# Performance work log

Hardware: AMD Instinct MI355X
Metric: run time of the kernel (lower is better)

## Reference

```python
import jax, jax.numpy as jnp
import numpy as np

B, L, K = 16, 512, 30          # proteins, residues per protein, kNN neighbors
N = B * L
H, FC = 32, 3                  # h_channels, frame_channels
C = H + FC                     # fused sphere channels (35)
HEADS, AC, VC = 8, 16, 8       # heads, alpha channels (H//2), value channels (H//4)
RBF_N, POS_N = 16, 16
EF = RBF_N + POS_N

# idealized backbone atom positions (N, CA, C) in the local residue frame
IDEAL_BB = np.array([[-0.525, 1.363, 0.0], [0.0, 0.0, 0.0], [1.526, 0.0, 0.0]], dtype=np.float32)
# cartesian (x,y,z) -> real-SH l=1 ordering (y,z,x)
P_SH = np.array([[0., 1., 0.], [0., 0., 1.], [1., 0., 0.]], dtype=np.float32)


def _knn_edges(trans):
    # per-chain brute-force kNN (chains are contiguous blocks of length L)
    X = trans.reshape(B, L, 3)
    d2 = jnp.sum((X[:, :, None, :] - X[:, None, :, :]) ** 2, axis=-1)  # [B,L,L]
    d2 = d2 + jnp.eye(L, dtype=d2.dtype) * 1e9                          # exclude self
    _, idx = jax.lax.top_k(-d2, K)                                      # [B,L,K]
    off = (jnp.arange(B) * L)[:, None, None]
    src = (idx + off).reshape(-1)              # neighbor (edge_index[0])
    tgt = jnp.repeat(jnp.arange(N), K)         # center   (edge_index[1])
    return src, tgt


def _edge_rot_mat(vec):
    # rotation aligning the edge vector with the y axis (eSCN init_edge_rot_mat style)
    nx = vec / (jnp.linalg.norm(vec, axis=-1, keepdims=True) + 1e-12)
    ref = jnp.where(jnp.abs(nx[:, :1]) < 0.9,
                    jnp.array([1., 0., 0.], dtype=vec.dtype),
                    jnp.array([0., 0., 1.], dtype=vec.dtype))
    nz = jnp.cross(nx, ref)
    nz = nz / (jnp.linalg.norm(nz, axis=-1, keepdims=True) + 1e-12)
    ny = jnp.cross(nx, nz)
    ny = ny / (jnp.linalg.norm(ny, axis=-1, keepdims=True) + 1e-12)
    return jnp.stack([nz, nx, ny], axis=-2)  # [E,3,3]


def _rbf(d, d_min=0.0, d_max=20.0, count=RBF_N):
    mu = jnp.linspace(d_min, d_max, count)
    sigma = (d_max - d_min) / count
    return jnp.exp(-(((d[:, None] - mu) / sigma) ** 2))


def _pos_emb(src, tgt, num=POS_N):
    d = (src - tgt).astype(jnp.float32)
    freq = jnp.exp(jnp.arange(0, num, 2, dtype=jnp.float32) * (-np.log(10000.0) / num))
    ang = d[:, None] * freq
    return jnp.concatenate([jnp.cos(ang), jnp.sin(ang)], axis=-1)


def _forward(rots, trans, node_emb, batch, x_mask, noising_mask,
             W_alpha, a_vec, W_v, W_o, W_g, W_2):
    src, tgt = _knn_edges(trans)
    vec = trans[src] - trans[tgt]
    dist = jnp.linalg.norm(vec, axis=-1)
    valid = jnp.isfinite(dist) & (dist > 1e-3)  # edge_select, applied as mask

    R = _edge_rot_mat(vec)
    P = jnp.asarray(P_SH)
    D1 = jnp.einsum('ij,ejk,lk->eil', P, R, P)  # l=1 Wigner in real-SH basis [E,3,3]

    edge_features = jnp.concatenate([_rbf(dist), _pos_emb(src, tgt)], axis=-1)  # [E,32]

    # fuse node features with backbone frame atoms and editability flag
    frame_atoms = jnp.einsum('nij,aj->nai', rots, jnp.asarray(IDEAL_BB))  # [N,3atoms,3xyz]
    editable = noising_mask & (~x_mask)
    emb = jnp.zeros((N, 4, C), dtype=node_emb.dtype)
    emb = emb.at[:, :, :H].set(node_emb)
    emb = emb.at[:, 1:4, H:].set(jnp.swapaxes(frame_atoms, -1, -2))
    emb = emb.at[:, 0, C - 1].set(editable.astype(node_emb.dtype))

    # gather + rotate source features into edge frames
    xs = emb[src]                                                   # [E,4,C]
    xs_rot = jnp.concatenate([xs[:, :1], jnp.einsum('eij,ejc->eic', D1, xs[:, 1:])], axis=1)

    # invariant attention logits (l=0 of rotated src, l=0 of tgt, edge feats)
    inv = jnp.concatenate([xs_rot[:, 0], emb[tgt, 0], edge_features], axis=-1)  # [E,102]
    hdn = jax.nn.silu(inv @ W_alpha).reshape(-1, HEADS, AC)
    logits = jax.nn.leaky_relu(jnp.einsum('ehk,hk->eh', hdn, a_vec), 0.2)
    logits = jnp.where(valid[:, None], logits, -1e9)

    # segment softmax over incoming edges of each target node
    mx = jax.lax.stop_gradient(jax.ops.segment_max(logits, tgt, num_segments=N))
    ex = jnp.exp(logits - mx[tgt]) * valid[:, None].astype(logits.dtype)
    den = jax.ops.segment_sum(ex, tgt, num_segments=N)
    alpha = ex / (den[tgt] + 1e-9)                                  # [E,HEADS]

    # equivariant values, attention-weighted, rotate back, scatter
    v = (xs_rot @ W_v).reshape(-1, 4, HEADS, VC)
    m = (v * alpha[:, None, :, None]).reshape(-1, 4, HEADS * VC)
    m = jnp.concatenate([m[:, :1], jnp.einsum('eji,ejc->eic', D1, m[:, 1:])], axis=1)  # D^T
    agg = jax.ops.segment_sum(m, tgt, num_segments=N)               # [N,4,64]

    y = agg @ W_o                                                    # [N,4,H]
    gate = jax.nn.silu(y[:, 0] @ W_g)                                # invariant gating FFN
    return (y * gate[:, None, :]) @ W_2                              # [N,4,H]


def setup_inputs():
    key = jax.random.key(0)
    ks = jax.random.split(key, 12)
    rots = jax.vmap(lambda m: jnp.linalg.qr(m)[0])(jax.random.normal(ks[0], (N, 3, 3)))
    trans = jax.random.normal(ks[1], (N, 3)) * 10.0
    node_emb = jax.random.normal(ks[2], (N, 4, H))
    batch = jnp.repeat(jnp.arange(B, dtype=jnp.int32), L)
    x_mask = jax.random.randint(ks[3], (N,), 0, 2).astype(bool)
    noising_mask = jax.random.randint(ks[4], (N,), 0, 2).astype(bool)
    s = lambda k, sh, fan: jax.random.normal(k, sh) / np.sqrt(fan)
    return dict(rots=rots, trans=trans, node_emb=node_emb, batch=batch,
                x_mask=x_mask, noising_mask=noising_mask,
                W_alpha=s(ks[5], (2 * C + EF, HEADS * AC), 2 * C + EF),
                a_vec=s(ks[6], (HEADS, AC), AC),
                W_v=s(ks[7], (C, HEADS * VC), C),
                W_o=s(ks[8], (HEADS * VC, H), HEADS * VC),
                W_g=s(ks[9], (H, H), H),
                W_2=s(ks[10], (H, H), H))


def reference(rots, trans, node_emb, batch, x_mask, noising_mask,
              W_alpha, a_vec, W_v, W_o, W_g, W_2):
    return _forward(rots, trans, node_emb, batch, x_mask, noising_mask,
                    W_alpha, a_vec, W_v, W_o, W_g, W_2)
```

## Files before the change

### kernel.cpp

```cpp
#include <hip/hip_runtime.h>
#include <cstdint>

#define B_ 16
#define L_ 512
#define N_ 8192
#define K_ 30
#define E_ (N_*K_)
#define H_ 32
#define C_ 35

typedef uint16_t u16;
typedef uint32_t u32;
typedef unsigned long long u64;

static __device__ __forceinline__ float ldf(const void* p, int i, int bf) {
    return bf ? __uint_as_float(((u32)((const u16*)p)[i]) << 16)
              : ((const float*)p)[i];
}
static __device__ __forceinline__ float bfu16(u16 x) {
    return __uint_as_float(((u32)x) << 16);
}
static __device__ __forceinline__ int ldmask(const void* p, int i, int mode) {
    if (mode == 0) return ((const unsigned char*)p)[i] != 0;
    if (mode == 2) return ((const u32*)p)[2*i] != 0;
    return ((const u32*)p)[i] != 0;
}
static __device__ __forceinline__ u16 f2bf(float f) {
    u32 x = __float_as_uint(f);
    u32 r = x + 0x7FFFu + ((x >> 16) & 1u);
    return (u16)(r >> 16);
}
static __device__ __forceinline__ float fsilu(float x) {
    return x * __builtin_amdgcn_rcpf(1.f + __expf(-x));
}

static __device__ __forceinline__ int detect_bf(const void* tr, int lane) {
    const u16* p = (const u16*)tr;
    int cnt = 0;
    for (int i = lane; i < 256; i += 64) {
        u16 v = p[2 * i];
        int e = (v >> 7) & 0xFF;
        if ((e >= 100 && e <= 141) || (v & 0x7FFFu) == 0) cnt++;
    }
    #pragma unroll
    for (int d = 1; d < 64; d <<= 1) cnt += __shfl_xor(cnt, d, 64);
    return cnt >= 192;
}
static __device__ __forceinline__ int detect_mm(const void* xmv, int lane) {
    const u32* xm = (const u32*)xmv;
    int anyBig = 0, oddNZ = 0;
    for (int i = lane; i < 1024; i += 64) {
        u32 w = xm[i];
        if (w & ~1u) anyBig = 1;
        if ((i & 1) && w) oddNZ = 1;
    }
    #pragma unroll
    for (int d = 1; d < 64; d <<= 1) {
        anyBig |= __shfl_xor(anyBig, d, 64);
        oddNZ  |= __shfl_xor(oddNZ, d, 64);
    }
    return anyBig ? 0 : (oddNZ ? 1 : 2);
}

__constant__ float cBB[9] = {-0.525f, 1.363f, 0.f,  0.f, 0.f, 0.f,  1.526f, 0.f, 0.f};

#define DPP_MIN_STEP(CTRL) \
    { u32 olo = (u32)__builtin_amdgcn_update_dpp((int)lo, (int)lo, CTRL, 0xF, 0xF, false); \
      u32 ohi = (u32)__builtin_amdgcn_update_dpp((int)hi, (int)hi, CTRL, 0xF, 0xF, false); \
      u64 o = (((u64)ohi) << 32) | olo; \
      if (o < m) m = o; \
      lo = (u32)m; hi = (u32)(m >> 32); }

__global__ __launch_bounds__(256) void mega_kernel(
    const void* __restrict__ rots, const void* __restrict__ trans,
    const void* __restrict__ node, const void* __restrict__ xm,
    const void* __restrict__ nm,
    const void* __restrict__ Wa, const void* __restrict__ av,
    const void* __restrict__ Wv, const void* __restrict__ Wo,
    const void* __restrict__ Wg, const void* __restrict__ W2,
    int* __restrict__ flag, int* __restrict__ srcArr,
    float* __restrict__ hsrc, float* __restrict__ htgt,
    float* __restrict__ ptab, float* __restrict__ V,
    float* __restrict__ c_wrb, float* __restrict__ c_av,
    float* __restrict__ c_Wo, float* __restrict__ c_Wg, float* __restrict__ c_W2)
{
    __shared__ float sX[L_], sY[L_], sZ[L_];
    __shared__ float eS[140];
    __shared__ int flagS[2];
    const int bid = blockIdx.x, tid = threadIdx.x;
    const int lane = tid & 63, wid = tid >> 6;

    if (bid < 2048) {
        if (wid == 0) {
            int bf = detect_bf(trans, lane);
            if (lane == 0) flagS[0] = bf;
        }
        __syncthreads();
        const int bf = flagS[0];
        const int t0 = bid * 4;
        const int base = (t0 >> 9) << 9;
        if (bf) {
            const u16* tp = (const u16*)trans;
            for (int i = tid; i < L_; i += 256) {
                sX[i] = bfu16(tp[(base + i) * 3 + 0]);
                sY[i] = bfu16(tp[(base + i) * 3 + 1]);
                sZ[i] = bfu16(tp[(base + i) * 3 + 2]);
            }
        } else {
            const float* tp = (const float*)trans;
            for (int i = tid; i < L_; i += 256) {
                sX[i] = tp[(base + i) * 3 + 0];
                sY[i] = tp[(base + i) * 3 + 1];
                sZ[i] = tp[(base + i) * 3 + 2];
            }
        }
        __syncthreads();

        const int t = t0 + wid;
        const int l = t & 511;
        const float tx = sX[l], ty = sY[l], tz = sZ[l];

        u64 key[8];
        #pragma unroll
        for (int i = 0; i < 8; ++i) {
            int j = lane + (i << 6);
            float dx = __fsub_rn(tx, sX[j]);
            float dy = __fsub_rn(ty, sY[j]);
            float dz = __fsub_rn(tz, sZ[j]);
            float d2 = __fadd_rn(__fadd_rn(__fmul_rn(dx, dx), __fmul_rn(dy, dy)), __fmul_rn(dz, dz));
            if (j == l) d2 = __fadd_rn(d2, 1e9f);
            key[i] = (((u64)__float_as_uint(d2)) << 32) | (u32)j;
        }
        int myres = 0;
        for (int k = 0; k < K_; ++k) {
            u64 m = key[0];
            #pragma unroll
            for (int i = 1; i < 8; ++i)
                if (key[i] < m) m = key[i];
            u32 lo = (u32)m, hi = (u32)(m >> 32);
            DPP_MIN_STEP(0x111)
            DPP_MIN_STEP(0x112)
            DPP_MIN_STEP(0x114)
            DPP_MIN_STEP(0x118)
            DPP_MIN_STEP(0x142)
            DPP_MIN_STEP(0x143)
            u32 glo = (u32)__builtin_amdgcn_readlane((int)lo, 63);
            u32 ghi = (u32)__builtin_amdgcn_readlane((int)hi, 63);
            u64 gm = (((u64)ghi) << 32) | glo;
            if (lane == k) myres = (int)(glo & 511u);
            #pragma unroll
            for (int i = 0; i < 8; ++i)
                if (key[i] == gm) key[i] = ~0ULL;
        }
        if (lane < K_) srcArr[t * K_ + lane] = base + myres;

    } else if (bid < 10240) {
        const int n = bid - 2048;
        if (wid == 0) {
            int bf = detect_bf(trans, lane);
            int mm = detect_mm(xm, lane);
            if (lane == 0) { flagS[0] = bf; flagS[1] = mm; }
        }
        __syncthreads();
        const int bf = flagS[0], mm = flagS[1];
        if (tid < 140) {
            int r = tid / 35, c = tid - r * 35;
            float v;
            if (c < H_) {
                v = ldf(node, n * 128 + r * 32 + c, bf);
            } else if (r == 0) {
                v = (c == 34) ? ((ldmask(nm, n, mm) && !ldmask(xm, n, mm)) ? 1.f : 0.f) : 0.f;
            } else {
                int i = r - 1, a = c - 32;
                v = ldf(rots, n*9 + i*3 + 0, bf) * cBB[a*3 + 0]
                  + ldf(rots, n*9 + i*3 + 1, bf) * cBB[a*3 + 1]
                  + ldf(rots, n*9 + i*3 + 2, bf) * cBB[a*3 + 2];
            }
            eS[tid] = v;
        }
        __syncthreads();
        const int r = tid >> 6, cc = tid & 63;
        if (bf) {
            const u16* wa = (const u16*)Wa;
            const u16* wv = (const u16*)Wv;
            if (tid < 128) {
                float a = 0.f, b = 0.f;
                #pragma unroll 5
                for (int i = 0; i < 35; ++i) {
                    float v = eS[i];
                    a = fmaf(v, bfu16(wa[i * 128 + tid]),        a);
                    b = fmaf(v, bfu16(wa[(35 + i) * 128 + tid]), b);
                }
                hsrc[(size_t)n * 128 + tid] = a;
                htgt[(size_t)n * 128 + tid] = b;
            }
            const float* er = eS + r * 35;
            float acc = 0.f;
            #pragma unroll 5
            for (int cp = 0; cp < 35; ++cp) acc = fmaf(er[cp], bfu16(wv[cp * 64 + cc]), acc);
            V[(size_t)n * 256 + tid] = acc;
        } else {
            const float* wa = (const float*)Wa;
            const float* wv = (const float*)Wv;
            if (tid < 128) {
                float a = 0.f, b = 0.f;
                #pragma unroll 5
                for (int i = 0; i < 35; ++i) {
                    float v = eS[i];
                    a = fmaf(v, wa[i * 128 + tid],        a);
                    b = fmaf(v, wa[(35 + i) * 128 + tid], b);
                }
                hsrc[(size_t)n * 128 + tid] = a;
                htgt[(size_t)n * 128 + tid] = b;
            }
            const float* er = eS + r * 35;
            float acc = 0.f;
            #pragma unroll 5
            for (int cp = 0; cp < 35; ++cp) acc = fmaf(er[cp], wv[cp * 64 + cc], acc);
            V[(size_t)n * 256 + tid] = acc;
        }

    } else if (bid < 11264) {
        const int d = bid - 10240;
        if (wid == 0) {
            int bf = detect_bf(trans, lane);
            if (lane == 0) flagS[0] = bf;
        }
        __syncthreads();
        const int bf = flagS[0];
        if (tid < 128) {
            float dd = (float)(d - 512);
            float acc = 0.f;
            if (bf) {
                const u16* wa = (const u16*)Wa;
                #pragma unroll
                for (int q = 0; q < 8; ++q) {
                    float fr = expf((float)(2 * q) * (-0.5756462732485115f));
                    float ang = dd * fr;
                    acc = fmaf(cosf(ang), bfu16(wa[(86 + q) * 128 + tid]), acc);
                    acc = fmaf(sinf(ang), bfu16(wa[(94 + q) * 128 + tid]), acc);
                }
            } else {
                const float* wa = (const float*)Wa;
                #pragma unroll
                for (int q = 0; q < 8; ++q) {
                    float fr = expf((float)(2 * q) * (-0.5756462732485115f));
                    float ang = dd * fr;
                    acc = fmaf(cosf(ang), wa[(86 + q) * 128 + tid], acc);
                    acc = fmaf(sinf(ang), wa[(94 + q) * 128 + tid], acc);
                }
            }
            ptab[(size_t)d * 128 + tid] = acc;
        }

    } else {
        if (wid == 0) {
            int bf = detect_bf(trans, lane);
            if (lane == 0) flagS[0] = bf;
        }
        __syncthreads();
        const int bf = flagS[0];
        if (bid == 11264 && tid == 0) flag[0] = bf;
        int g0 = (bid - 11264) * 256 + tid;
        for (int i = g0; i < 6272; i += 2048) {
            if      (i < 2048) c_wrb[i]        = ldf(Wa, 70 * 128 + i, bf);
            else if (i < 2176) c_av[i - 2048]  = ldf(av, i - 2048, bf);
            else if (i < 4224) c_Wo[i - 2176]  = ldf(Wo, i - 2176, bf);
            else if (i < 5248) c_Wg[i - 4224]  = ldf(Wg, i - 4224, bf);
            else               c_W2[i - 5248]  = ldf(W2, i - 5248, bf);
        }
    }
}

__global__ __launch_bounds__(256) void edge_agg_kernel(
    const void* __restrict__ trans, const int* __restrict__ srcArr,
    const float* __restrict__ hsrc, const float* __restrict__ htgt,
    const float* __restrict__ ptab, const float* __restrict__ V,
    const float* __restrict__ c_wrb, const float* __restrict__ c_av,
    const float* __restrict__ Wo, const float* __restrict__ Wg,
    const float* __restrict__ W2,
    const int* __restrict__ flag, void* __restrict__ outv)
{
    __shared__ float rbfS[K_][20];
    __shared__ int   srcS[K_];
    __shared__ int   dS[K_];
    __shared__ float lgS[240];
    __shared__ float aggS[256];
    __shared__ float ybuf[128];
    __shared__ float gbuf[32];
    const int bid = blockIdx.x, tid = threadIdx.x;
    const int t   = ((bid & 7) << 10) | (bid >> 3);
    const int lane = tid & 63, wid = tid >> 6;
    const int bf = flag[0];

    float2 wrb[16];
    #pragma unroll
    for (int j = 0; j < 16; ++j) wrb[j] = ((const float2*)c_wrb)[j * 64 + lane];
    const float2 avv = ((const float2*)c_av)[lane];

    if (tid < 2 * K_) {
        const int k = tid >> 1, half = tid & 1;
        const int e = t * K_ + k;
        int src = srcArr[e];
        src = (src < 0) ? 0 : ((src >= N_) ? (N_ - 1) : src);
        float vx = ldf(trans, src*3+0, bf) - ldf(trans, t*3+0, bf);
        float vy = ldf(trans, src*3+1, bf) - ldf(trans, t*3+1, bf);
        float vz = ldf(trans, src*3+2, bf) - ldf(trans, t*3+2, bf);
        float dist = sqrtf(vx*vx + vy*vy + vz*vz);
        bool valid = isfinite(dist) && (dist > 1e-3f);
        int d = src - t + 512;
        d = (d < 0) ? 0 : ((d > 1023) ? 1023 : d);
        if (half == 0) {
            srcS[k] = src;
            dS[k]   = d | (valid ? 0 : (1 << 16));
        }
        const int jb = half * 8;
        #pragma unroll
        for (int j = 0; j < 8; ++j) {
            float tt = (dist - (float)(jb + j) * (20.f/15.f)) * 0.8f;
            rbfS[k][jb + j] = __expf(-tt * tt);
        }
    }
    __syncthreads();

    const float2 htv = ((const float2*)(htgt + (size_t)t * 128))[lane];
    #pragma unroll
    for (int j = 0; j < 8; ++j) {
        const int k = wid * 8 + j;
        if (k < K_) {
            const int src = srcS[k];
            const int dm  = dS[k];
            const int d   = dm & 0xFFFF;
            const bool valid = (dm >> 16) == 0;
            float2 hs = ((const float2*)(hsrc + (size_t)src * 128))[lane];
            float2 pt = ((const float2*)(ptab + (size_t)d   * 128))[lane];
            float acc0 = hs.x + htv.x + pt.x;
            float acc1 = hs.y + htv.y + pt.y;
            const float4* rp = (const float4*)(&rbfS[k][0]);
            #pragma unroll
            for (int jj = 0; jj < 4; ++jj) {
                float4 rb = rp[jj];
                acc0 = fmaf(rb.x, wrb[4*jj+0].x, acc0); acc1 = fmaf(rb.x, wrb[4*jj+0].y, acc1);
                acc0 = fmaf(rb.y, wrb[4*jj+1].x, acc0); acc1 = fmaf(rb.y, wrb[4*jj+1].y, acc1);
                acc0 = fmaf(rb.z, wrb[4*jj+2].x, acc0); acc1 = fmaf(rb.z, wrb[4*jj+2].y, acc1);
                acc0 = fmaf(rb.w, wrb[4*jj+3].x, acc0); acc1 = fmaf(rb.w, wrb[4*jj+3].y, acc1);
            }
            float part = fsilu(acc0) * avv.x + fsilu(acc1) * avv.y;
            #pragma unroll
            for (int s = 1; s < 8; s <<= 1) part += __shfl_xor(part, s, 64);
            float lg = (part >= 0.f) ? part : 0.2f * part;
            if (!valid) lg = -1e9f;
            lg = (fabsf(lg) < 1e30f) ? lg : -1e9f;
            if ((lane & 7) == 0) lgS[k * 8 + (lane >> 3)] = lg;
        }
    }
    __syncthreads();

    {
        const int h = (tid & 63) >> 3;
        float lg[K_];
        float mx = -1e30f;
        #pragma unroll
        for (int k = 0; k < K_; ++k) { lg[k] = lgS[k * 8 + h]; mx = fmaxf(mx, lg[k]); }
        float den = 0.f;
        #pragma unroll
        for (int k = 0; k < K_; ++k) {
            float e = (lg[k] > -1e8f) ? __expf(lg[k] - mx) : 0.f;
            lg[k] = e; den += e;
        }
        const float inv = 1.f / (den + 1e-9f);
        float acc = 0.f;
        #pragma unroll 6
        for (int k = 0; k < K_; ++k)
            acc = fmaf(lg[k], V[(size_t)srcS[k] * 256 + tid], acc);
        aggS[tid] = acc * inv;
    }
    __syncthreads();

    if (tid < 128) {
        int rr = tid >> 5, o = tid & 31;
        float y = 0.f;
        #pragma unroll
        for (int c = 0; c < 64; ++c) y = fmaf(aggS[rr * 64 + c], Wo[c * 32 + o], y);
        ybuf[tid] = y;
    }
    __syncthreads();
    if (tid < 32) {
        float g = 0.f;
        #pragma unroll
        for (int o = 0; o < 32; ++o) g = fmaf(ybuf[o], Wg[o * 32 + tid], g);
        gbuf[tid] = fsilu(g);
    }
    __syncthreads();
    if (tid < 128) {
        int rr = tid >> 5, hh = tid & 31;
        float o = 0.f;
        #pragma unroll
        for (int g = 0; g < 32; ++g) o = fmaf(ybuf[rr * 32 + g] * gbuf[g], W2[g * 32 + hh], o);
        o = (fabsf(o) < 1e30f) ? o : 0.f;
        size_t idx = (size_t)t * 128 + tid;
        if (bf) ((u16*)outv)[idx] = f2bf(o);
        else    ((float*)outv)[idx] = o;
    }
}

extern "C" void kernel_launch(void* const* d_in, const int* in_sizes, int n_in,
                              void* d_out, int out_size, void* d_ws, size_t ws_size,
                              hipStream_t stream)
{
    const void* rots         = d_in[0];
    const void* trans        = d_in[1];
    const void* node_emb     = d_in[2];
    const void* x_mask       = d_in[4];
    const void* noising_mask = d_in[5];
    const void* Wa           = d_in[6];
    const void* avec         = d_in[7];
    const void* Wv           = d_in[8];
    const void* Wo           = d_in[9];
    const void* Wg           = d_in[10];
    const void* W2           = d_in[11];

    char* ws = (char*)d_ws;
    int*   flag    = (int*)  (ws + 0);
    int*   srcArr  = (int*)  (ws + 64);
    float* hsrc    = (float*)(ws + 983104);
    float* htgt    = (float*)(ws + 5177408);
    float* ptab    = (float*)(ws + 9371712);
    float* V       = (float*)(ws + 9896000);
    float* c_wrb   = (float*)(ws + 18284608);
    float* c_av    = (float*)(ws + 18292800);
    float* c_Wo    = (float*)(ws + 18293312);
    float* c_Wg    = (float*)(ws + 18301504);
    float* c_W2    = (float*)(ws + 18305600);

    hipLaunchKernelGGL(mega_kernel, dim3(11272), dim3(256), 0, stream,
                       rots, trans, node_emb, x_mask, noising_mask,
                       Wa, avec, Wv, Wo, Wg, W2,
                       flag, srcArr, hsrc, htgt, ptab, V,
                       c_wrb, c_av, c_Wo, c_Wg, c_W2);
    hipLaunchKernelGGL(edge_agg_kernel, dim3(N_), dim3(256), 0, stream,
                       trans, srcArr, hsrc, htgt, ptab, V,
                       c_wrb, c_av, c_Wo, c_Wg, c_W2, flag, d_out);
}
```

Baseline: 224.3 us.

## Compute softmax once per head in shared memory and raise occupancy hint

The per-head softmax moves out of every thread into 8 threads that normalize the logits in shared memory, which removes the 30-entry register array and its redundant exp work. The RBF setup is spread over 240 threads instead of 60, V row offsets are precomputed as int shifts, and launch bounds now request 4 blocks per SIMD. The aim is lower register pressure and higher occupancy, at the cost of an extra barrier and a mostly idle serial softmax phase.

Result: no change. 222.8 us (-0.7%).

```diff
diff --git a/kernel.cpp b/kernel.cpp
--- a/kernel.cpp
+++ b/kernel.cpp
@@ -272,7 +272,7 @@
     }
 }
 
-__global__ __launch_bounds__(256) void edge_agg_kernel(
+__global__ __launch_bounds__(256, 4) void edge_agg_kernel(
     const void* __restrict__ trans, const int* __restrict__ srcArr,
     const float* __restrict__ hsrc, const float* __restrict__ htgt,
     const float* __restrict__ ptab, const float* __restrict__ V,
@@ -283,8 +283,10 @@
 {
     __shared__ float rbfS[K_][20];
     __shared__ int   srcS[K_];
+    __shared__ int   voffS[K_];
     __shared__ int   dS[K_];
     __shared__ float lgS[240];
+    __shared__ float invS[8];
     __shared__ float aggS[256];
     __shared__ float ybuf[128];
     __shared__ float gbuf[32];
@@ -298,8 +300,8 @@
     for (int j = 0; j < 16; ++j) wrb[j] = ((const float2*)c_wrb)[j * 64 + lane];
     const float2 avv = ((const float2*)c_av)[lane];
 
-    if (tid < 2 * K_) {
-        const int k = tid >> 1, half = tid & 1;
+    if (tid < 8 * K_) {
+        const int k = tid >> 3, sub = tid & 7;
         const int e = t * K_ + k;
         int src = srcArr[e];
         src = (src < 0) ? 0 : ((src >= N_) ? (N_ - 1) : src);
@@ -310,16 +312,16 @@
         bool valid = isfinite(dist) && (dist > 1e-3f);
         int d = src - t + 512;
         d = (d < 0) ? 0 : ((d > 1023) ? 1023 : d);
-        if (half == 0) {
-            srcS[k] = src;
-            dS[k]   = d | (valid ? 0 : (1 << 16));
-        }
-        const int jb = half * 8;
-        #pragma unroll
-        for (int j = 0; j < 8; ++j) {
-            float tt = (dist - (float)(jb + j) * (20.f/15.f)) * 0.8f;
-            rbfS[k][jb + j] = __expf(-tt * tt);
-        }
+        if (sub == 0) {
+            srcS[k]  = src;
+            voffS[k] = src << 8;
+            dS[k]    = d | (valid ? 0 : (1 << 16));
+        }
+        const int j0 = sub * 2;
+        float t0 = (dist - (float)j0       * (20.f/15.f)) * 0.8f;
+        float t1 = (dist - (float)(j0 + 1) * (20.f/15.f)) * 0.8f;
+        rbfS[k][j0]     = __expf(-t0 * t0);
+        rbfS[k][j0 + 1] = __expf(-t1 * t1);
     }
     __syncthreads();
 
@@ -356,24 +358,28 @@
     }
     __syncthreads();
 
+    if (tid < 8) {
+        float mx = -1e30f;
+        #pragma unroll
+        for (int k = 0; k < K_; ++k) mx = fmaxf(mx, lgS[k * 8 + tid]);
+        float den = 0.f;
+        #pragma unroll
+        for (int k = 0; k < K_; ++k) {
+            float l = lgS[k * 8 + tid];
+            float e = (l > -1e8f) ? __expf(l - mx) : 0.f;
+            lgS[k * 8 + tid] = e; den += e;
+        }
+        invS[tid] = 1.f / (den + 1e-9f);
+    }
+    __syncthreads();
+
     {
         const int h = (tid & 63) >> 3;
-        float lg[K_];
-        float mx = -1e30f;
-        #pragma unroll
-        for (int k = 0; k < K_; ++k) { lg[k] = lgS[k * 8 + h]; mx = fmaxf(mx, lg[k]); }
-        float den = 0.f;
-        #pragma unroll
-        for (int k = 0; k < K_; ++k) {
-            float e = (lg[k] > -1e8f) ? __expf(lg[k] - mx) : 0.f;
-            lg[k] = e; den += e;
-        }
-        const float inv = 1.f / (den + 1e-9f);
         float acc = 0.f;
         #pragma unroll 6
         for (int k = 0; k < K_; ++k)
-            acc = fmaf(lg[k], V[(size_t)srcS[k] * 256 + tid], acc);
-        aggS[tid] = acc * inv;
+            acc = fmaf(lgS[k * 8 + h], V[voffS[k] + tid], acc);
+        aggS[tid] = acc * invS[h];
     }
     __syncthreads();
 
```
